# Optimization experiments

Measured on AMD Instinct MI355X. Metric: run time of the kernel, lower is better.

Reference implementation:

```python
import jax, jax.numpy as jnp
import numpy as np

N_BLOCK = 3
N_NODES = 20000
N_EDGES = 320000
N_GRAPHS = 200
F = 128          # n_hidden_feat = n_GCN_feat
FE = 3 * F       # concat [ni, nj, delta]
K1 = 36          # N_shbf * N_srbf
K2 = 26          # plane-wave feature dim (hard-coded in source)


def setup_inputs() -> dict:
    key = jax.random.key(0)
    ks = jax.random.split(key, 20)
    s = 0.05
    inp = {
        "nodes": jax.random.normal(ks[0], (N_NODES, F), jnp.float32),
        "edge_sources": jax.random.randint(ks[1], (N_EDGES,), 0, N_NODES),
        "edge_targets": jax.random.randint(ks[2], (N_EDGES,), 0, N_NODES),
        # keep distances away from 0 to avoid blowing up (nj-ni)/rij
        "edge_distance": jax.random.uniform(ks[3], (N_EDGES,), jnp.float32, 0.5, 1.5),
        "graph_indices": jax.random.randint(ks[4], (N_NODES,), 0, N_GRAPHS),
        "node_counts": jnp.ones((N_GRAPHS,), jnp.float32) * (N_NODES / N_GRAPHS),
        "combine_sets": jax.random.normal(ks[5], (N_EDGES, K1), jnp.float32),
        "plane_wave": jax.random.normal(ks[6], (N_EDGES, K2), jnp.float32),
        # parameters ([in, out] layout; torch Linear has bias=False here)
        "W_emb": jax.random.normal(ks[7], (F, F), jnp.float32) * s,
        "Wg": jax.random.normal(ks[8], (N_BLOCK, FE, F), jnp.float32) * s,
        "Wm": jax.random.normal(ks[9], (N_BLOCK, FE, F), jnp.float32) * s,
        "W1v": jax.random.normal(ks[10], (N_BLOCK, K1, F), jnp.float32) * s,
        "W2v": jax.random.normal(ks[11], (N_BLOCK, K2, F), jnp.float32) * s,
        "W2vg": jax.random.normal(ks[12], (N_BLOCK, K2, F), jnp.float32) * s,
        "Wp1": jax.random.normal(ks[13], (N_BLOCK, F, F), jnp.float32) * s,
        "Wp2": jax.random.normal(ks[14], (N_BLOCK, F, F), jnp.float32) * s,
        "Wpsi": jax.random.normal(ks[15], (N_BLOCK, F, F), jnp.float32) * s,
        "Wlr1": jax.random.normal(ks[16], (F, F // 2), jnp.float32) * s,
        "Wlr2": jax.random.normal(ks[17], (F // 2, F // 3), jnp.float32) * s,
        "Wlr3": jax.random.normal(ks[18], (F // 3, 1), jnp.float32) * s,
    }
    return inp


def reference(nodes, edge_sources, edge_targets, edge_distance, graph_indices,
              node_counts, combine_sets, plane_wave,
              W_emb, Wg, Wm, W1v, W2v, W2vg, Wp1, Wp2, Wpsi, Wlr1, Wlr2, Wlr3):
    G = node_counts.shape[0]
    # NodeEmbedding: Linear + Sigmoid
    x = jax.nn.sigmoid(nodes @ W_emb)
    pools = []
    for i in range(N_BLOCK):
        # GatedGraphConvolution: edge gather -> concat -> gated MLP -> scatter-add
        ni = x[edge_sources]                      # [E, F]
        nj = x[edge_targets]                      # [E, F]
        delta = (nj - ni) / edge_distance[:, None]
        fe = jnp.concatenate([ni, nj, delta], axis=1)   # [E, 3F]
        e_gate = jax.nn.sigmoid(fe @ Wg[i])
        e_mlp = jax.nn.elu(fe @ Wm[i])
        z1 = combine_sets @ W1v[i]                # note: linear1_vector_gate unused in source forward
        z2 = (plane_wave @ W2v[i]) * jax.nn.sigmoid(plane_wave @ W2vg[i])
        z = e_gate * e_mlp * (z1 + z2)            # [E, F]
        x = x.at[edge_sources].add(z)             # output = input.clone(); index_add_
        # Gated_pooling (division by node_counts is discarded in the source -> plain segment sum)
        zp = jax.nn.elu(x @ Wp1[i])
        pools.append(jax.ops.segment_sum(zp * (x @ Wp2[i]), graph_indices, num_segments=G))
        # MLP_psi2n
        x = jax.nn.elu(x @ Wpsi[i])
    out = pools[0] + pools[1] + pools[2]          # sum over blocks, [G, F]
    out = jax.nn.elu(out @ Wlr1)
    out = jax.nn.elu(out @ Wlr2)
    out = out @ Wlr3                              # [G, 1]
    return out.squeeze()
```

## Files before the change

kernel.cpp:

```cpp
#include <hip/hip_runtime.h>
#include <math.h>

#define NNODES 20000
#define NEDGES 320000
#define NGRAPHS 200
#define K1 36
#define K2 26

struct WPtrs { const float* w[6]; };

__device__ __forceinline__ float sigf(float v) { return 1.0f / (1.0f + expf(-v)); }
__device__ __forceinline__ float eluf(float v) { return v > 0.0f ? v : expm1f(v); }

__device__ __forceinline__ float fsig(float v) { return __builtin_amdgcn_rcpf(1.0f + __expf(-v)); }
__device__ __forceinline__ float felu(float v) { return v > 0.0f ? v : __expf(v) - 1.0f; }

__global__ __launch_bounds__(256) void gemm128_kernel(
    const float* __restrict__ A, WPtrs wp, float* __restrict__ out,
    int out_stride, int act)
{
    __shared__ float4 Wl[2048];
    __shared__ float4 Al[2048];

    const int half  = blockIdx.y & 1;
    const int chunk = blockIdx.y >> 1;
    const float4* W4 = (const float4*)(wp.w[chunk] + half * 64);

    for (int idx = threadIdx.x; idx < 2048; idx += 256) {
        int k = idx >> 4, fq = idx & 15;
        Wl[idx] = W4[k * 32 + fq];
    }
    const int m0 = blockIdx.x * 64;
    const float4* A4 = (const float4*)A;
    for (int idx = threadIdx.x; idx < 2048; idx += 256) {
        int r = idx >> 5, k4 = idx & 31;
        int row = m0 + r;
        Al[idx] = (row < NNODES) ? A4[(size_t)row * 32 + k4] : make_float4(0.f, 0.f, 0.f, 0.f);
    }
    __syncthreads();

    const int fg = threadIdx.x & 15;
    const int ng = threadIdx.x >> 4;

    float acc[4][4] = {};
    #pragma unroll 4
    for (int k4 = 0; k4 < 32; ++k4) {
        float4 a[4], w[4];
        #pragma unroll
        for (int j = 0; j < 4; ++j) a[j] = Al[(ng * 4 + j) * 32 + k4];
        #pragma unroll
        for (int q = 0; q < 4; ++q) w[q] = Wl[(k4 * 4 + q) * 16 + fg];
        #pragma unroll
        for (int j = 0; j < 4; ++j) {
            const float* ap = (const float*)&a[j];
            #pragma unroll
            for (int q = 0; q < 4; ++q) {
                const float* wq = (const float*)&w[q];
                #pragma unroll
                for (int jj = 0; jj < 4; ++jj)
                    acc[j][jj] = fmaf(ap[q], wq[jj], acc[j][jj]);
            }
        }
    }

    const int coff = chunk * 128 + half * 64 + fg * 4;
    #pragma unroll
    for (int j = 0; j < 4; ++j) {
        int row = m0 + ng * 4 + j;
        if (row < NNODES) {
            float4 v; float* vp = (float*)&v;
            #pragma unroll
            for (int jj = 0; jj < 4; ++jj) {
                float t = acc[j][jj];
                vp[jj] = act ? sigf(t) : t;
            }
            *(float4*)(out + (size_t)row * out_stride + coff) = v;
        }
    }
}

__global__ __launch_bounds__(256, 2) void edge_kernel(
    const float* __restrict__ P,
    const int* __restrict__ esrc, const int* __restrict__ etgt,
    const float* __restrict__ dist,
    const float* __restrict__ cs, const float* __restrict__ pw,
    const float* __restrict__ W1v, const float* __restrict__ W2v,
    const float* __restrict__ W2vg,
    float* __restrict__ x)
{
    const int f    = threadIdx.x & 127;
    const int esub = threadIdx.x >> 7;

    float w1[K1], w2[K2], w2g[K2];
    #pragma unroll
    for (int k = 0; k < K1; ++k) w1[k]  = W1v[k * 128 + f];
    #pragma unroll
    for (int k = 0; k < K2; ++k) w2[k]  = W2v[k * 128 + f];
    #pragma unroll
    for (int k = 0; k < K2; ++k) w2g[k] = W2vg[k * 128 + f];
    #pragma unroll
    for (int k = 0; k < K1; ++k) asm volatile("" : "+v"(w1[k]));
    #pragma unroll
    for (int k = 0; k < K2; ++k) asm volatile("" : "+v"(w2[k]));
    #pragma unroll
    for (int k = 0; k < K2; ++k) asm volatile("" : "+v"(w2g[k]));

    const int base = blockIdx.x * 64 + esub * 4;

    for (int it = 0; it < 8; ++it) {
        const int e0 = __builtin_amdgcn_readfirstlane(base + it * 8);

        int s[4], t[4];
        float dd[4];
        #pragma unroll
        for (int u = 0; u < 4; ++u) {
            s[u]  = esrc[e0 + u];
            t[u]  = etgt[e0 + u];
            dd[u] = dist[e0 + u];
        }

        float g0[4], g1[4], g2t[4], g2s[4], m0[4], m1[4], m2t[4], m2s[4];
        #pragma unroll
        for (int u = 0; u < 4; ++u) {
            const float* Ps = P + (size_t)s[u] * 768;
            const float* Pt = P + (size_t)t[u] * 768;
            g0[u]  = Ps[f];
            g2s[u] = Ps[256 + f];
            m0[u]  = Ps[384 + f];
            m2s[u] = Ps[640 + f];
            g1[u]  = Pt[128 + f];
            g2t[u] = Pt[256 + f];
            m1[u]  = Pt[512 + f];
            m2t[u] = Pt[640 + f];
        }

        float z1[4] = {}, za[4] = {}, zb[4] = {};
        #pragma unroll
        for (int k = 0; k < K1; ++k) {
            const float wv = w1[k];
            #pragma unroll
            for (int u = 0; u < 4; ++u)
                z1[u] = fmaf(cs[(size_t)(e0 + u) * K1 + k], wv, z1[u]);
        }
        #pragma unroll
        for (int k = 0; k < K2; ++k) {
            const float wa = w2[k], wb = w2g[k];
            #pragma unroll
            for (int u = 0; u < 4; ++u) {
                const float p = pw[(size_t)(e0 + u) * K2 + k];
                za[u] = fmaf(p, wa, za[u]);
                zb[u] = fmaf(p, wb, zb[u]);
            }
        }

        #pragma unroll
        for (int u = 0; u < 4; ++u) {
            const float invd = __builtin_amdgcn_rcpf(dd[u]);
            const float g = g0[u] + g1[u] + (g2t[u] - g2s[u]) * invd;
            const float m = m0[u] + m1[u] + (m2t[u] - m2s[u]) * invd;
            const float z = fsig(g) * felu(m) * (z1[u] + za[u] * fsig(zb[u]));
            atomicAdd(x + (size_t)s[u] * 128 + f, z);
        }
    }
}

__global__ __launch_bounds__(256) void pool_psi_kernel(
    const float* __restrict__ T, const int* __restrict__ gidx,
    float* __restrict__ pools, float* __restrict__ xout)
{
    int idx = blockIdx.x * 256 + threadIdx.x;
    int n = idx >> 7, f = idx & 127;
    float h1 = eluf(T[(size_t)n * 384 + f]);
    float h2 = T[(size_t)n * 384 + 128 + f];
    atomicAdd(pools + (size_t)gidx[n] * 128 + f, h1 * h2);
    xout[(size_t)n * 128 + f] = eluf(T[(size_t)n * 384 + 256 + f]);
}

__global__ __launch_bounds__(64) void final_kernel(
    const float* __restrict__ pools,
    const float* __restrict__ Wlr1, const float* __restrict__ Wlr2,
    const float* __restrict__ Wlr3, float* __restrict__ out)
{
    __shared__ float h1[64];
    __shared__ float h2[42];
    const int g = blockIdx.x;
    const int f = threadIdx.x;

    float a = 0.f;
    #pragma unroll 8
    for (int k = 0; k < 128; ++k) a = fmaf(pools[(size_t)g * 128 + k], Wlr1[k * 64 + f], a);
    h1[f] = eluf(a);
    __syncthreads();
    if (f < 42) {
        float b = 0.f;
        #pragma unroll
        for (int k = 0; k < 64; ++k) b = fmaf(h1[k], Wlr2[k * 42 + f], b);
        h2[f] = eluf(b);
    }
    __syncthreads();
    if (f == 0) {
        float c = 0.f;
        #pragma unroll
        for (int k = 0; k < 42; ++k) c = fmaf(h2[k], Wlr3[k], c);
        out[g] = c;
    }
}

__global__ void zero_kernel(float* p, int n)
{
    int i = blockIdx.x * 256 + threadIdx.x;
    if (i < n) p[i] = 0.f;
}

extern "C" void kernel_launch(void* const* d_in, const int* in_sizes, int n_in,
                              void* d_out, int out_size, void* d_ws, size_t ws_size,
                              hipStream_t stream)
{
    const float* nodes = (const float*)d_in[0];
    const int*   esrc  = (const int*)d_in[1];
    const int*   etgt  = (const int*)d_in[2];
    const float* dist  = (const float*)d_in[3];
    const int*   gidx  = (const int*)d_in[4];
    const float* cs    = (const float*)d_in[6];
    const float* pw    = (const float*)d_in[7];
    const float* W_emb = (const float*)d_in[8];
    const float* Wg    = (const float*)d_in[9];
    const float* Wm    = (const float*)d_in[10];
    const float* W1v   = (const float*)d_in[11];
    const float* W2v   = (const float*)d_in[12];
    const float* W2vg  = (const float*)d_in[13];
    const float* Wp1   = (const float*)d_in[14];
    const float* Wp2   = (const float*)d_in[15];
    const float* Wpsi  = (const float*)d_in[16];
    const float* Wlr1  = (const float*)d_in[17];
    const float* Wlr2  = (const float*)d_in[18];
    const float* Wlr3  = (const float*)d_in[19];
    float* outp = (float*)d_out;

    float* xA    = (float*)d_ws;
    float* xB    = xA + (size_t)NNODES * 128;
    float* P     = xB + (size_t)NNODES * 128;
    float* pools = P + (size_t)NNODES * 768;

    zero_kernel<<<100, 256, 0, stream>>>(pools, NGRAPHS * 128);

    {
        WPtrs wp{}; wp.w[0] = W_emb;
        gemm128_kernel<<<dim3(313, 2), 256, 0, stream>>>(nodes, wp, xA, 128, 1);
    }

    float* xc = xA;
    float* xn = xB;
    for (int i = 0; i < 3; ++i) {
        WPtrs wp{};
        const float* Wgi = Wg + (size_t)i * 49152;
        const float* Wmi = Wm + (size_t)i * 49152;
        wp.w[0] = Wgi;          wp.w[1] = Wgi + 16384;  wp.w[2] = Wgi + 32768;
        wp.w[3] = Wmi;          wp.w[4] = Wmi + 16384;  wp.w[5] = Wmi + 32768;
        gemm128_kernel<<<dim3(313, 12), 256, 0, stream>>>(xc, wp, P, 768, 0);

        edge_kernel<<<5000, 256, 0, stream>>>(P, esrc, etgt, dist, cs, pw,
            W1v + (size_t)i * (K1 * 128),
            W2v + (size_t)i * (K2 * 128),
            W2vg + (size_t)i * (K2 * 128), xc);

        WPtrs wq{};
        wq.w[0] = Wp1 + (size_t)i * 16384;
        wq.w[1] = Wp2 + (size_t)i * 16384;
        wq.w[2] = Wpsi + (size_t)i * 16384;
        gemm128_kernel<<<dim3(313, 6), 256, 0, stream>>>(xc, wq, P, 384, 0);

        pool_psi_kernel<<<10000, 256, 0, stream>>>(P, gidx, pools, xn);

        float* tmp = xc; xc = xn; xn = tmp;
    }

    final_kernel<<<NGRAPHS, 64, 0, stream>>>(pools, Wlr1, Wlr2, Wlr3, outp);
}
```

Measured before the change: 1.280 ms.

## Sort edges by source via counting sort and merge same-source atomics

Builds a per-call counting sort of edges by source node (histogram, scan, scatter into a permutation) and has the edge kernel walk edges in that order. Consecutive edges sharing a source are summed in registers before a single atomicAdd, cutting atomic traffic and improving locality of the scatter target. Edge weights move from per-thread registers to shared memory, and blocks grow to 512 threads. The cost is extra sort kernels per call, indirect gathers of cs/pw/dist through the permutation, and atomic ordering that no longer matches the original edge order.

Measured after the change: 1.678 ms. +31.1%, slower.

```diff
diff --git a/kernel.cpp b/kernel.cpp
--- a/kernel.cpp
+++ b/kernel.cpp
@@ -6,6 +6,7 @@
 #define NGRAPHS 200
 #define K1 36
 #define K2 26
+#define NBINS 20480
 
 struct WPtrs { const float* w[6]; };
 
@@ -79,8 +80,50 @@
     }
 }
 
-__global__ __launch_bounds__(256, 2) void edge_kernel(
-    const float* __restrict__ P,
+__global__ void hist_kernel(const int* __restrict__ esrc, int* __restrict__ cnt)
+{
+    int i = blockIdx.x * 256 + threadIdx.x;
+    if (i < NEDGES) atomicAdd(&cnt[esrc[i]], 1);
+}
+
+__global__ __launch_bounds__(1024) void scan_kernel(
+    const int* __restrict__ cnt, int* __restrict__ cursor)
+{
+    __shared__ int ps[1024];
+    const int t = threadIdx.x;
+    const int b0 = t * 20;
+    int sum = 0;
+    #pragma unroll
+    for (int b = 0; b < 20; ++b) sum += cnt[b0 + b];
+    ps[t] = sum;
+    __syncthreads();
+    for (int off = 1; off < 1024; off <<= 1) {
+        int v = (t >= off) ? ps[t - off] : 0;
+        __syncthreads();
+        ps[t] += v;
+        __syncthreads();
+    }
+    int acc = ps[t] - sum;
+    #pragma unroll
+    for (int b = 0; b < 20; ++b) {
+        int c = cnt[b0 + b];
+        cursor[b0 + b] = acc;
+        acc += c;
+    }
+}
+
+__global__ void scatter_kernel(const int* __restrict__ esrc,
+                               int* __restrict__ cursor, int* __restrict__ eperm)
+{
+    int i = blockIdx.x * 256 + threadIdx.x;
+    if (i < NEDGES) {
+        int p = atomicAdd(&cursor[esrc[i]], 1);
+        eperm[p] = i;
+    }
+}
+
+__global__ __launch_bounds__(512, 4) void edge_kernel(
+    const float* __restrict__ P, const int* __restrict__ eperm,
     const int* __restrict__ esrc, const int* __restrict__ etgt,
     const float* __restrict__ dist,
     const float* __restrict__ cs, const float* __restrict__ pw,
@@ -88,35 +131,29 @@
     const float* __restrict__ W2vg,
     float* __restrict__ x)
 {
-    const int f    = threadIdx.x & 127;
+    __shared__ float wl[(K1 + 2 * K2) * 128];
+
+    const int f = threadIdx.x & 127;
+    for (int idx = threadIdx.x; idx < K1 * 128; idx += 512) wl[idx] = W1v[idx];
+    for (int idx = threadIdx.x; idx < K2 * 128; idx += 512) wl[K1 * 128 + idx] = W2v[idx];
+    for (int idx = threadIdx.x; idx < K2 * 128; idx += 512) wl[(K1 + K2) * 128 + idx] = W2vg[idx];
+    __syncthreads();
+
     const int esub = threadIdx.x >> 7;
-
-    float w1[K1], w2[K2], w2g[K2];
-    #pragma unroll
-    for (int k = 0; k < K1; ++k) w1[k]  = W1v[k * 128 + f];
-    #pragma unroll
-    for (int k = 0; k < K2; ++k) w2[k]  = W2v[k * 128 + f];
-    #pragma unroll
-    for (int k = 0; k < K2; ++k) w2g[k] = W2vg[k * 128 + f];
-    #pragma unroll
-    for (int k = 0; k < K1; ++k) asm volatile("" : "+v"(w1[k]));
-    #pragma unroll
-    for (int k = 0; k < K2; ++k) asm volatile("" : "+v"(w2[k]));
-    #pragma unroll
-    for (int k = 0; k < K2; ++k) asm volatile("" : "+v"(w2g[k]));
-
     const int base = blockIdx.x * 64 + esub * 4;
 
-    for (int it = 0; it < 8; ++it) {
-        const int e0 = __builtin_amdgcn_readfirstlane(base + it * 8);
-
-        int s[4], t[4];
+    #pragma unroll 1
+    for (int it = 0; it < 4; ++it) {
+        const int j0 = base + it * 16;
+
+        int e[4], s[4], t[4];
         float dd[4];
         #pragma unroll
         for (int u = 0; u < 4; ++u) {
-            s[u]  = esrc[e0 + u];
-            t[u]  = etgt[e0 + u];
-            dd[u] = dist[e0 + u];
+            e[u] = __builtin_amdgcn_readfirstlane(eperm[j0 + u]);
+            s[u] = __builtin_amdgcn_readfirstlane(esrc[e[u]]);
+            t[u] = __builtin_amdgcn_readfirstlane(etgt[e[u]]);
+            dd[u] = dist[e[u]];
         }
 
         float g0[4], g1[4], g2t[4], g2s[4], m0[4], m1[4], m2t[4], m2s[4];
@@ -137,30 +174,43 @@
         float z1[4] = {}, za[4] = {}, zb[4] = {};
         #pragma unroll
         for (int k = 0; k < K1; ++k) {
-            const float wv = w1[k];
+            const float wv = wl[k * 128 + f];
             #pragma unroll
             for (int u = 0; u < 4; ++u)
-                z1[u] = fmaf(cs[(size_t)(e0 + u) * K1 + k], wv, z1[u]);
+                z1[u] = fmaf(cs[(size_t)e[u] * K1 + k], wv, z1[u]);
         }
         #pragma unroll
         for (int k = 0; k < K2; ++k) {
-            const float wa = w2[k], wb = w2g[k];
+            const float wa = wl[(K1 + k) * 128 + f];
+            const float wb = wl[(K1 + K2 + k) * 128 + f];
             #pragma unroll
             for (int u = 0; u < 4; ++u) {
-                const float p = pw[(size_t)(e0 + u) * K2 + k];
+                const float p = pw[(size_t)e[u] * K2 + k];
                 za[u] = fmaf(p, wa, za[u]);
                 zb[u] = fmaf(p, wb, zb[u]);
             }
         }
 
+        float z[4];
         #pragma unroll
         for (int u = 0; u < 4; ++u) {
             const float invd = __builtin_amdgcn_rcpf(dd[u]);
             const float g = g0[u] + g1[u] + (g2t[u] - g2s[u]) * invd;
             const float m = m0[u] + m1[u] + (m2t[u] - m2s[u]) * invd;
-            const float z = fsig(g) * felu(m) * (z1[u] + za[u] * fsig(zb[u]));
-            atomicAdd(x + (size_t)s[u] * 128 + f, z);
-        }
+            z[u] = fsig(g) * felu(m) * (z1[u] + za[u] * fsig(zb[u]));
+        }
+
+        float acc = z[0];
+        #pragma unroll
+        for (int u = 1; u < 4; ++u) {
+            if (s[u] == s[u - 1]) {
+                acc += z[u];
+            } else {
+                atomicAdd(x + (size_t)s[u - 1] * 128 + f, acc);
+                acc = z[u];
+            }
+        }
+        atomicAdd(x + (size_t)s[3] * 128 + f, acc);
     }
 }
 
@@ -241,8 +291,16 @@
     float* xB    = xA + (size_t)NNODES * 128;
     float* P     = xB + (size_t)NNODES * 128;
     float* pools = P + (size_t)NNODES * 768;
+    int* cnt     = (int*)(pools + NGRAPHS * 128);
+    int* cursor  = cnt + NBINS;
+    int* eperm   = cursor + NBINS;
 
     zero_kernel<<<100, 256, 0, stream>>>(pools, NGRAPHS * 128);
+
+    zero_kernel<<<(NBINS + 255) / 256, 256, 0, stream>>>((float*)cnt, NBINS);
+    hist_kernel<<<(NEDGES + 255) / 256, 256, 0, stream>>>(esrc, cnt);
+    scan_kernel<<<1, 1024, 0, stream>>>(cnt, cursor);
+    scatter_kernel<<<(NEDGES + 255) / 256, 256, 0, stream>>>(esrc, cursor, eperm);
 
     {
         WPtrs wp{}; wp.w[0] = W_emb;
@@ -259,7 +317,7 @@
         wp.w[3] = Wmi;          wp.w[4] = Wmi + 16384;  wp.w[5] = Wmi + 32768;
         gemm128_kernel<<<dim3(313, 12), 256, 0, stream>>>(xc, wp, P, 768, 0);
 
-        edge_kernel<<<5000, 256, 0, stream>>>(P, esrc, etgt, dist, cs, pw,
+        edge_kernel<<<5000, 512, 0, stream>>>(P, eperm, esrc, etgt, dist, cs, pw,
             W1v + (size_t)i * (K1 * 128),
             W2v + (size_t)i * (K2 * 128),
             W2vg + (size_t)i * (K2 * 128), xc);
```
